# Kernel tuning notes

Hardware: AMD Instinct MI355X
Metric: run time of the kernel (lower is better)

Reference implementation:

```python
import jax, jax.numpy as jnp
import numpy as np

B = 2048   # jets (graphs)
P = 50     # particles per jet
N = B * P  # nodes
E = B * P * P  # within-jet all-pairs radius-graph edges (incl. self-loops)
H = 5      # edge-MLP width ([5,5,5,5] channel list)
EPS = 1e-5
NEG_SLOPE = 0.01


def _batchnorm(h, gamma, beta):
    # training-mode batch norm over the edge dimension (biased variance, as torch)
    mu = jnp.mean(h, axis=0)
    var = jnp.mean(h * h, axis=0) - mu * mu
    return gamma * (h - mu) * jax.lax.rsqrt(var + EPS) + beta


def setup_inputs() -> dict:
    key = jax.random.key(0)
    ks = jax.random.split(key, 16)
    # angles: per-jet center offset + tight spread so all within-jet pairs are inside dR=0.4
    centers = jax.random.normal(ks[0], (B, 1, 2), dtype=jnp.float32) + jnp.array([2.0, 0.5], dtype=jnp.float32)
    angles = (centers + 0.1 * jax.random.normal(ks[1], (B, P, 2), dtype=jnp.float32)).reshape(N, 2)
    pt = jax.random.uniform(ks[2], (N,), dtype=jnp.float32, minval=0.1, maxval=1.0)
    features = jnp.linalg.norm(angles, axis=-1, keepdims=True)  # rho = |view_as_complex(angles)|, [N,1]
    # radius graph: with the tight spread every within-jet pair is within dR -> fixed E
    ii = np.arange(P)
    pi, pj = np.meshgrid(ii, ii, indexing='ij')
    base = (np.arange(B, dtype=np.int64) * P)[:, None]
    src = (base + pj.ravel()[None, :]).ravel()  # x_j (source)
    dst = (base + pi.ravel()[None, :]).ravel()  # x_i (target) = aggregation index
    edge_index = jnp.asarray(np.stack([src, dst]), dtype=jnp.int32)  # [2, E]
    def lin(k, o, i):
        return (jax.random.normal(k, (o, i), dtype=jnp.float32) / np.sqrt(i)).astype(jnp.float32)
    W1 = lin(ks[3], H, 5); b1 = jnp.zeros((H,), jnp.float32)
    W2 = lin(ks[4], H, H); b2 = jnp.zeros((H,), jnp.float32)
    W3 = lin(ks[5], H, H); b3 = jnp.zeros((H,), jnp.float32)
    g1 = jnp.ones((H,), jnp.float32); bt1 = jnp.zeros((H,), jnp.float32)
    g2 = jnp.ones((H,), jnp.float32); bt2 = jnp.zeros((H,), jnp.float32)
    return {"pt": pt, "features": features, "angles": angles,
            "W1": W1, "b1": b1, "g1": g1, "bt1": bt1,
            "W2": W2, "b2": b2, "g2": g2, "bt2": bt2,
            "W3": W3, "b3": b3, "edge_index": edge_index}


def reference(pt, features, angles, W1, b1, g1, bt1, W2, b2, g2, bt2, W3, b3, edge_index):
    src = edge_index[0]  # j (source)
    dst = edge_index[1]  # i (target, aggregation index)
    x = jnp.concatenate([pt[:, None], features, angles], axis=1)  # [N, 4]
    xi = x[dst]  # [E, 4]
    xj = x[src]
    # complex ratio angles_i / angles_j in real arithmetic
    ar, ai = xi[:, 2], xi[:, 3]
    br, bi = xj[:, 2], xj[:, 3]
    den = br * br + bi * bi
    dr = (ar * br + ai * bi) / den
    di = (ai * br - ar * bi) / den
    fi = xi[:, 1:2]
    fj = xj[:, 1:2]
    mlp_in = jnp.concatenate([fi, fj, fj - fi, dr[:, None], di[:, None]], axis=1)  # [E, 5]
    h = jax.nn.leaky_relu(_batchnorm(mlp_in @ W1.T + b1, g1, bt1), NEG_SLOPE)
    h = jax.nn.leaky_relu(_batchnorm(h @ W2.T + b2, g2, bt2), NEG_SLOPE)
    h = h @ W3.T + b3  # [E, 5]
    msg = jnp.concatenate([xi[:, :1], h, xi[:, 2:4]], axis=1)  # [E, 8]
    pt_e = msg[:, 0]
    denom = jax.ops.segment_sum(pt_e, dst, num_segments=N)  # [N]
    wj = pt_e / denom[dst]
    agg = jax.ops.segment_sum(wj[:, None] * msg, dst, num_segments=N)  # [N, 8]
    # exp(2*pi*i*theta) * z with theta = agg[:, -3], z = complex(agg[:, -2:])
    theta = agg[:, 5]
    zr, zi = agg[:, 6], agg[:, 7]
    c = jnp.cos(2.0 * jnp.pi * theta)
    s = jnp.sin(2.0 * jnp.pi * theta)
    out = jnp.concatenate([agg[:, :5], (c * zr - s * zi)[:, None], (c * zi + s * zr)[:, None]], axis=1)  # [N, 7]
    return out
```

## Files before the change

### kernel.cpp

```cpp
#include <hip/hip_runtime.h>

#define PP 50
#define TPB 256
#define NBATCH 2048
#define GB 2
#define NBLK2 (NBATCH / GB)
#define NBLK1 512
#define NCOPY 64
#define NSLOT 30

static constexpr float EPSF = 1e-5f;
static constexpr double INV_ETOT = 1.0 / 5120000.0;

static __device__ __forceinline__ float lrelu(float x) {
    return fmaxf(x, 0.01f * x);
}
static __device__ __forceinline__ float rfl(float x) {
    return __int_as_float(__builtin_amdgcn_readfirstlane(__float_as_int(x)));
}


__global__ __launch_bounds__(TPB) void stats1_kernel(
    const float* __restrict__ feat, const float* __restrict__ ang,
    const float* __restrict__ W1, const float* __restrict__ b1,
    double* __restrict__ acc)
{
    __shared__ double bacc[4][10];
    const int t = threadIdx.x;
    const int lane = t & 63;
    const int wv = t >> 6;

    float v0[5], v1[5], v2[5], v3[5], bb1[5];
#pragma unroll
    for (int o = 0; o < 5; ++o) {
        v0[o] = rfl(W1[o*5+0] - W1[o*5+2]);
        v1[o] = rfl(W1[o*5+1] + W1[o*5+2]);
        v2[o] = rfl(W1[o*5+3]);
        v3[o] = rfl(W1[o*5+4]);
        bb1[o] = rfl(b1[o]);
    }

    float f = 0.f, zr = 0.f, zi = 0.f, inv = 0.f;
    if (lane < PP) {
        const int idx = (blockIdx.x * 4 + wv) * PP + lane;
        f = feat[idx];
        float2 a2 = ((const float2*)ang)[idx];
        zr = a2.x; zi = a2.y;
        inv = 1.0f / (zr*zr + zi*zi);
    }
    const float wr = zr * inv, wi = -zi * inv;

    float p[16] = { f, f*f, zr, zi, wr, wi, f*zr, f*zi, f*wr, f*wi,
                    zr*zr, zi*zi, zr*zi, wr*wr, wi*wi, wr*wi };
#pragma unroll
    for (int k = 0; k < 16; ++k) {
        float v = p[k];
#pragma unroll
        for (int off = 32; off > 0; off >>= 1) v += __shfl_down(v, off, 64);
        p[k] = v;
    }
    if (lane == 0) {
        const double P0 = p[0], P1 = p[1], P2 = p[2], P3 = p[3], P4 = p[4];
        const double P5 = p[5], P6 = p[6], P7 = p[7], P8 = p[8], P9 = p[9];
        const double P10 = p[10], P11 = p[11], P12 = p[12];
        const double P13 = p[13], P14 = p[14], P15 = p[15];
        const double Sfi = 50.0 * P0;
        const double Sdr = P2*P4 - P3*P5;
        const double Sdi = P3*P4 + P2*P5;
        const double m00 = 50.0 * P1, m11 = m00, m01 = P0*P0;
        const double m02 = P6*P4 - P7*P5;
        const double m03 = P7*P4 + P6*P5;
        const double m12 = P2*P8 - P3*P9;
        const double m13 = P3*P8 + P2*P9;
        const double m22 = P10*P13 - 2.0*P12*P15 + P11*P14;
        const double m33 = P11*P13 + 2.0*P12*P15 + P10*P14;
        const double m23 = P12*P13 + P10*P15 - P11*P15 - P12*P14;
#pragma unroll
        for (int o = 0; o < 5; ++o) {
            const double a0=v0[o], a1=v1[o], a2=v2[o], a3=v3[o], bo=bb1[o];
            const double sy = a0*Sfi + a1*Sfi + a2*Sdr + a3*Sdi + 2500.0*bo;
            const double q  = a0*a0*m00 + a1*a1*m11 + a2*a2*m22 + a3*a3*m33
                           + 2.0*(a0*a1*m01 + a0*a2*m02 + a0*a3*m03
                                + a1*a2*m12 + a1*a3*m13 + a2*a3*m23);
            bacc[wv][o]   = sy;
            bacc[wv][5+o] = q + 2.0*bo*sy - 2500.0*bo*bo;
        }
    }
    __syncthreads();
    if (t < 10) {
        double s = bacc[0][t] + bacc[1][t] + bacc[2][t] + bacc[3][t];
        atomicAdd(&acc[t * NCOPY + (blockIdx.x & (NCOPY-1))], s);
    }
}

__global__ __launch_bounds__(TPB, 2) void pass2_kernel(
    const float* __restrict__ feat, const float* __restrict__ ang,
    const float* __restrict__ W1, const float* __restrict__ b1,
    const float* __restrict__ g1, const float* __restrict__ bt1,
    double* __restrict__ acc)
{
    __shared__ float4 nd[GB * PP];
    __shared__ float4 ndj[GB * PP];
    __shared__ double tmp[10];
    __shared__ float red[4][20];
    const int t = threadIdx.x;

    if (t < GB * PP) {
        const int idx = blockIdx.x * (GB * PP) + t;
        float f = feat[idx];
        float2 a2 = ((const float2*)ang)[idx];
        float inv = 1.0f / (a2.x*a2.x + a2.y*a2.y);
        nd[t]  = make_float4(f, a2.x, a2.y, 0.0f);
        ndj[t] = make_float4(f, a2.x * inv, a2.y * inv, 0.0f);
    } else if (t >= 128 && t < 138) {
        const int k = t - 128;
        double s = 0.0;
#pragma unroll
        for (int c = 0; c < NCOPY; ++c) s += acc[k * NCOPY + c];
        tmp[k] = s;
    }

    float v0[5], v1[5], v2[5], v3[5], bb1[5];
#pragma unroll
    for (int o = 0; o < 5; ++o) {
        v0[o] = rfl(W1[o*5+0] - W1[o*5+2]);
        v1[o] = rfl(W1[o*5+1] + W1[o*5+2]);
        v2[o] = rfl(W1[o*5+3]);
        v3[o] = rfl(W1[o*5+4]);
        bb1[o] = rfl(b1[o]);
    }

    __syncthreads();

#pragma unroll
    for (int o = 0; o < 5; ++o) {
        double mu  = tmp[o]   * INV_ETOT;
        double var = tmp[5+o] * INV_ETOT - mu * mu;
        float sc = rfl(g1[o]) * rsqrtf((float)var + EPSF);
        float sh = rfl(rfl(bt1[o]) - (float)mu * sc);
        v0[o] = rfl(v0[o] * sc);
        v1[o] = rfl(v1[o] * sc);
        v2[o] = rfl(v2[o] * sc);
        v3[o] = rfl(v3[o] * sc);
        bb1[o] = rfl(fmaf(bb1[o], sc, sh));
    }

    float s1[5] = {0.f, 0.f, 0.f, 0.f, 0.f};
    float mm[15];
#pragma unroll
    for (int k = 0; k < 15; ++k) mm[k] = 0.f;

    if (t < 250) {
        const int pi = t / 5;
        const int s5 = t - pi*5;
#pragma unroll
        for (int g = 0; g < GB; ++g) {
            const float4 ni = nd[g*PP + pi];
            const float fi = ni.x, ari = ni.y, aii = ni.z;
            float4 njs[10];
#pragma unroll
            for (int q = 0; q < 10; ++q) njs[q] = ndj[g*PP + s5*10 + q];
#pragma unroll
            for (int q = 0; q < 10; ++q) {
                const float4 nj = njs[q];
                const float dr = fmaf(ari, nj.y,  aii*nj.z);
                const float di = fmaf(aii, nj.y, -ari*nj.z);
                float h1[5];
#pragma unroll
                for (int o = 0; o < 5; ++o) {
                    float y = fmaf(v0[o], fi, fmaf(v1[o], nj.x,
                              fmaf(v2[o], dr, fmaf(v3[o], di, bb1[o]))));
                    h1[o] = lrelu(y);
                }
#pragma unroll
                for (int k = 0; k < 5; ++k) {
                    s1[k] += h1[k];
#pragma unroll
                    for (int l = k; l < 5; ++l) {
                        const int idx = k*5 - (k*(k+1))/2 + l;
                        mm[idx] = fmaf(h1[k], h1[l], mm[idx]);
                    }
                }
            }
        }
    }

    float a[20];
#pragma unroll
    for (int k = 0; k < 5; ++k) a[k] = s1[k];
#pragma unroll
    for (int k = 0; k < 15; ++k) a[5+k] = mm[k];
#pragma unroll
    for (int k = 0; k < 20; ++k) {
        float v = a[k];
#pragma unroll
        for (int off = 32; off > 0; off >>= 1) v += __shfl_down(v, off, 64);
        a[k] = v;
    }
    const int lane = t & 63, wv = t >> 6;
    if (lane == 0) {
#pragma unroll
        for (int k = 0; k < 20; ++k) red[wv][k] = a[k];
    }
    __syncthreads();
    if (t < 20) {
        atomicAdd(&acc[(10 + t) * NCOPY + (blockIdx.x & (NCOPY-1))],
                  (double)(red[0][t] + red[1][t] + red[2][t] + red[3][t]));
    }
}

__global__ __launch_bounds__(TPB, 2) void pass3_kernel(
    const float* __restrict__ pt,
    const float* __restrict__ feat, const float* __restrict__ ang,
    const float* __restrict__ W1, const float* __restrict__ b1,
    const float* __restrict__ g1, const float* __restrict__ bt1,
    const float* __restrict__ W2, const float* __restrict__ b2,
    const float* __restrict__ g2, const float* __restrict__ bt2,
    const float* __restrict__ W3, const float* __restrict__ b3,
    const double* __restrict__ acc, float* __restrict__ out)
{
    __shared__ float4 nd[GB * PP];
    __shared__ float4 ndj[GB * PP];
    __shared__ float spt[GB * PP];
    __shared__ double tmp[NSLOT];
    __shared__ float scsh[4][5];
    __shared__ float part[250][5];
    const int t = threadIdx.x;

    if (t < GB * PP) {
        const int idx = blockIdx.x * (GB * PP) + t;
        float f = feat[idx];
        float2 a2 = ((const float2*)ang)[idx];
        float inv = 1.0f / (a2.x*a2.x + a2.y*a2.y);
        nd[t]  = make_float4(f, a2.x, a2.y, 0.0f);
        ndj[t] = make_float4(f, a2.x * inv, a2.y * inv, 0.0f);
        spt[t] = pt[idx];
    } else if (t >= 128 && t < 128 + NSLOT) {
        const int k = t - 128;
        double s = 0.0;
#pragma unroll
        for (int c = 0; c < NCOPY; ++c) s += acc[k * NCOPY + c];
        tmp[k] = s;
    }

    float v0[5], v1[5], v2[5], v3[5], bb1[5], w2[25], bb2[5], w3[25], bb3[5];
#pragma unroll
    for (int o = 0; o < 5; ++o) {
        v0[o] = rfl(W1[o*5+0] - W1[o*5+2]);
        v1[o] = rfl(W1[o*5+1] + W1[o*5+2]);
        v2[o] = rfl(W1[o*5+3]);
        v3[o] = rfl(W1[o*5+4]);
        bb1[o] = rfl(b1[o]); bb2[o] = rfl(b2[o]); bb3[o] = rfl(b3[o]);
    }
#pragma unroll
    for (int i = 0; i < 25; ++i) { w2[i] = rfl(W2[i]); w3[i] = rfl(W3[i]); }

    __syncthreads();

    if (t < 5) {
        const int o = t;
        double mu1  = tmp[o]   * INV_ETOT;
        double var1 = tmp[5+o] * INV_ETOT - mu1 * mu1;
        float sc1 = g1[o] * rsqrtf((float)var1 + EPSF);
        scsh[0][o] = sc1;
        scsh[1][o] = bt1[o] - (float)mu1 * sc1;

        double w[5], Sn[5];
#pragma unroll
        for (int k = 0; k < 5; ++k) {
            w[k]  = (double)w2[o*5+k];
            Sn[k] = tmp[10+k] * INV_ETOT;
        }
        double muw = 0.0;
#pragma unroll
        for (int k = 0; k < 5; ++k) muw += w[k] * Sn[k];
        double q = 0.0;
#pragma unroll
        for (int k = 0; k < 5; ++k) {
#pragma unroll
            for (int l = k; l < 5; ++l) {
                const int idx = k*5 - (k*(k+1))/2 + l;
                const double Mn = tmp[15+idx] * INV_ETOT;
                q += (k == l ? w[k]*w[k] : 2.0*w[k]*w[l]) * Mn;
            }
        }
        double var2 = q - muw * muw;
        double mu2  = muw + (double)bb2[o];
        float sc2 = g2[o] * rsqrtf((float)var2 + EPSF);
        scsh[2][o] = sc2;
        scsh[3][o] = bt2[o] - (float)mu2 * sc2;
    }
    __syncthreads();

#pragma unroll
    for (int o = 0; o < 5; ++o) {
        const float s1f = rfl(scsh[0][o]);
        const float s1h = rfl(scsh[1][o]);
        v0[o] = rfl(v0[o] * s1f);
        v1[o] = rfl(v1[o] * s1f);
        v2[o] = rfl(v2[o] * s1f);
        v3[o] = rfl(v3[o] * s1f);
        bb1[o] = rfl(fmaf(bb1[o], s1f, s1h));
        const float s2f = rfl(scsh[2][o]);
        const float s2h = rfl(scsh[3][o]);
#pragma unroll
        for (int k = 0; k < 5; ++k) w2[o*5+k] = rfl(w2[o*5+k] * s2f);
        bb2[o] = rfl(fmaf(bb2[o], s2f, s2h));
    }

    const int pi = t / 5;
    const int s5 = t - pi*5;

#pragma unroll
    for (int g = 0; g < GB; ++g) {
        float a[5] = {0.f, 0.f, 0.f, 0.f, 0.f};
        if (t < 250) {
            const float4 ni = nd[g*PP + pi];
            const float fi = ni.x, ari = ni.y, aii = ni.z;
            float4 njs[10];
#pragma unroll
            for (int q = 0; q < 10; ++q) njs[q] = ndj[g*PP + s5*10 + q];
#pragma unroll
            for (int q = 0; q < 10; ++q) {
                const float4 nj = njs[q];
                const float dr = fmaf(ari, nj.y,  aii*nj.z);
                const float di = fmaf(aii, nj.y, -ari*nj.z);
                float h1[5], h2[5];
#pragma unroll
                for (int o = 0; o < 5; ++o) {
                    float y = fmaf(v0[o], fi, fmaf(v1[o], nj.x,
                              fmaf(v2[o], dr, fmaf(v3[o], di, bb1[o]))));
                    h1[o] = lrelu(y);
                }
#pragma unroll
                for (int o = 0; o < 5; ++o) {
                    float y = bb2[o];
                    y = fmaf(w2[o*5+0], h1[0], y);
                    y = fmaf(w2[o*5+1], h1[1], y);
                    y = fmaf(w2[o*5+2], h1[2], y);
                    y = fmaf(w2[o*5+3], h1[3], y);
                    y = fmaf(w2[o*5+4], h1[4], y);
                    h2[o] = lrelu(y);
                }
#pragma unroll
                for (int o = 0; o < 5; ++o) a[o] += h2[o];
            }
#pragma unroll
            for (int c = 0; c < 5; ++c) part[t][c] = a[c];
        }
        __syncthreads();

        if (t < PP) {
            float hm[5];
#pragma unroll
            for (int c = 0; c < 5; ++c) {
                hm[c] = (part[5*t][c] + part[5*t+1][c] + part[5*t+2][c] +
                         part[5*t+3][c] + part[5*t+4][c]) * 0.02f;
            }
            float m[5];
#pragma unroll
            for (int c = 0; c < 5; ++c) {
                float y = bb3[c];
                y = fmaf(w3[c*5+0], hm[0], y);
                y = fmaf(w3[c*5+1], hm[1], y);
                y = fmaf(w3[c*5+2], hm[2], y);
                y = fmaf(w3[c*5+3], hm[3], y);
                y = fmaf(w3[c*5+4], hm[4], y);
                m[c] = y;
            }
            const int node = g*PP + t;
            const int d = blockIdx.x * (GB * PP) + node;
            const float4 ni = nd[node];
            float ss, cc;
            sincosf(6.2831853071795865f * m[4], &ss, &cc);
            float* o = out + (size_t)d * 7;
            o[0] = spt[node];
            o[1] = m[0];
            o[2] = m[1];
            o[3] = m[2];
            o[4] = m[3];
            o[5] = cc * ni.y - ss * ni.z;
            o[6] = cc * ni.z + ss * ni.y;
        }
        __syncthreads();
    }
}

extern "C" void kernel_launch(void* const* d_in, const int* in_sizes, int n_in,
                              void* d_out, int out_size, void* d_ws, size_t ws_size,
                              hipStream_t stream)
{
    const float* pt   = (const float*)d_in[0];
    const float* feat = (const float*)d_in[1];
    const float* ang  = (const float*)d_in[2];
    const float* W1   = (const float*)d_in[3];
    const float* b1   = (const float*)d_in[4];
    const float* g1   = (const float*)d_in[5];
    const float* bt1  = (const float*)d_in[6];
    const float* W2   = (const float*)d_in[7];
    const float* b2   = (const float*)d_in[8];
    const float* g2   = (const float*)d_in[9];
    const float* bt2  = (const float*)d_in[10];
    const float* W3   = (const float*)d_in[11];
    const float* b3   = (const float*)d_in[12];
    float* out = (float*)d_out;
    double* acc = (double*)d_ws;

    hipMemsetAsync(d_ws, 0, NSLOT * NCOPY * sizeof(double), stream);
    stats1_kernel<<<NBLK1, TPB, 0, stream>>>(feat, ang, W1, b1, acc);
    pass2_kernel<<<NBLK2, TPB, 0, stream>>>(feat, ang, W1, b1, g1, bt1, acc);
    pass3_kernel<<<NBLK2, TPB, 0, stream>>>(pt, feat, ang, W1, b1, g1, bt1, W2, b2,
                                            g2, bt2, W3, b3, acc, out);
}
```

Before: 140.5 us.

## Fuse three passes into one persistent kernel with grid-wide barriers

Merges the stats, second-moment and output kernels into a single kernel of 512 blocks, each handling four jets, and separates the phases with atomic grid barriers. Node data is staged in shared memory once and reused across all three phases instead of being reloaded per launch, and launch gaps disappear. It relies on all 512 blocks being co-resident (two per CU under the launch bounds); otherwise the spin barrier deadlocks. Fewer blocks also means less parallel slack in each phase.

```diff
diff --git a/kernel.cpp b/kernel.cpp
--- a/kernel.cpp
+++ b/kernel.cpp
@@ -3,10 +3,9 @@
 #define PP 50
 #define TPB 256
 #define NBATCH 2048
-#define GB 2
-#define NBLK2 (NBATCH / GB)
-#define NBLK1 512
-#define NCOPY 64
+#define GBF 4
+#define NBLKF (NBATCH / GBF)
+#define NCOPY 32
 #define NSLOT 30
 
 static constexpr float EPSF = 1e-5f;
@@ -18,17 +17,60 @@
 static __device__ __forceinline__ float rfl(float x) {
     return __int_as_float(__builtin_amdgcn_readfirstlane(__float_as_int(x)));
 }
-
-
-__global__ __launch_bounds__(TPB) void stats1_kernel(
+static __device__ __forceinline__ double aload(const double* p) {
+    return __hip_atomic_load(p, __ATOMIC_RELAXED, __HIP_MEMORY_SCOPE_AGENT);
+}
+
+static __device__ __forceinline__ void gbar(unsigned* cnt, unsigned* gen) {
+    __syncthreads();
+    if (threadIdx.x == 0) {
+        if (__hip_atomic_fetch_add(cnt, 1u, __ATOMIC_ACQ_REL,
+                                   __HIP_MEMORY_SCOPE_AGENT) == NBLKF - 1u) {
+            __hip_atomic_store(gen, 1u, __ATOMIC_RELEASE,
+                               __HIP_MEMORY_SCOPE_AGENT);
+        } else {
+            while (__hip_atomic_load(gen, __ATOMIC_ACQUIRE,
+                                     __HIP_MEMORY_SCOPE_AGENT) == 0u) {
+                __builtin_amdgcn_s_sleep(1);
+            }
+        }
+    }
+    __syncthreads();
+}
+
+__global__ __launch_bounds__(TPB, 2) void fused_kernel(
+    const float* __restrict__ pt,
     const float* __restrict__ feat, const float* __restrict__ ang,
     const float* __restrict__ W1, const float* __restrict__ b1,
-    double* __restrict__ acc)
+    const float* __restrict__ g1, const float* __restrict__ bt1,
+    const float* __restrict__ W2, const float* __restrict__ b2,
+    const float* __restrict__ g2, const float* __restrict__ bt2,
+    const float* __restrict__ W3, const float* __restrict__ b3,
+    double* __restrict__ acc, unsigned* __restrict__ bar,
+    float* __restrict__ out)
 {
+    __shared__ float4 nd[GBF * PP];
+    __shared__ float4 ndj[GBF * PP];
+    __shared__ float spt[GBF * PP];
     __shared__ double bacc[4][10];
+    __shared__ double tmp[NSLOT];
+    __shared__ float scsh[2][5];
+    __shared__ float red[4][20];
+    __shared__ float part[250][5];
+
     const int t = threadIdx.x;
     const int lane = t & 63;
     const int wv = t >> 6;
+
+    if (t < GBF * PP) {
+        const int idx = blockIdx.x * (GBF * PP) + t;
+        float f = feat[idx];
+        float2 a2 = ((const float2*)ang)[idx];
+        float inv = 1.0f / (a2.x * a2.x + a2.y * a2.y);
+        nd[t]  = make_float4(f, a2.x, a2.y, 0.0f);
+        ndj[t] = make_float4(f, a2.x * inv, a2.y * inv, 0.0f);
+        spt[t] = pt[idx];
+    }
 
     float v0[5], v1[5], v2[5], v3[5], bb1[5];
 #pragma unroll
@@ -40,96 +82,69 @@
         bb1[o] = rfl(b1[o]);
     }
 
-    float f = 0.f, zr = 0.f, zi = 0.f, inv = 0.f;
-    if (lane < PP) {
-        const int idx = (blockIdx.x * 4 + wv) * PP + lane;
-        f = feat[idx];
-        float2 a2 = ((const float2*)ang)[idx];
-        zr = a2.x; zi = a2.y;
-        inv = 1.0f / (zr*zr + zi*zi);
-    }
-    const float wr = zr * inv, wi = -zi * inv;
-
-    float p[16] = { f, f*f, zr, zi, wr, wi, f*zr, f*zi, f*wr, f*wi,
-                    zr*zr, zi*zi, zr*zi, wr*wr, wi*wi, wr*wi };
-#pragma unroll
-    for (int k = 0; k < 16; ++k) {
-        float v = p[k];
-#pragma unroll
-        for (int off = 32; off > 0; off >>= 1) v += __shfl_down(v, off, 64);
-        p[k] = v;
-    }
-    if (lane == 0) {
-        const double P0 = p[0], P1 = p[1], P2 = p[2], P3 = p[3], P4 = p[4];
-        const double P5 = p[5], P6 = p[6], P7 = p[7], P8 = p[8], P9 = p[9];
-        const double P10 = p[10], P11 = p[11], P12 = p[12];
-        const double P13 = p[13], P14 = p[14], P15 = p[15];
-        const double Sfi = 50.0 * P0;
-        const double Sdr = P2*P4 - P3*P5;
-        const double Sdi = P3*P4 + P2*P5;
-        const double m00 = 50.0 * P1, m11 = m00, m01 = P0*P0;
-        const double m02 = P6*P4 - P7*P5;
-        const double m03 = P7*P4 + P6*P5;
-        const double m12 = P2*P8 - P3*P9;
-        const double m13 = P3*P8 + P2*P9;
-        const double m22 = P10*P13 - 2.0*P12*P15 + P11*P14;
-        const double m33 = P11*P13 + 2.0*P12*P15 + P10*P14;
-        const double m23 = P12*P13 + P10*P15 - P11*P15 - P12*P14;
-#pragma unroll
-        for (int o = 0; o < 5; ++o) {
-            const double a0=v0[o], a1=v1[o], a2=v2[o], a3=v3[o], bo=bb1[o];
-            const double sy = a0*Sfi + a1*Sfi + a2*Sdr + a3*Sdi + 2500.0*bo;
-            const double q  = a0*a0*m00 + a1*a1*m11 + a2*a2*m22 + a3*a3*m33
-                           + 2.0*(a0*a1*m01 + a0*a2*m02 + a0*a3*m03
-                                + a1*a2*m12 + a1*a3*m13 + a2*a3*m23);
-            bacc[wv][o]   = sy;
-            bacc[wv][5+o] = q + 2.0*bo*sy - 2500.0*bo*bo;
-        }
-    }
-    __syncthreads();
+    __syncthreads();
+
+    {
+        float f = 0.f, zr = 0.f, zi = 0.f, wr = 0.f, wi = 0.f;
+        if (lane < PP) {
+            const int node = wv * PP + lane;
+            const float4 ni = nd[node];
+            const float4 nj = ndj[node];
+            f = ni.x; zr = ni.y; zi = ni.z;
+            wr = nj.y; wi = -nj.z;
+        }
+        float p[16] = { f, f*f, zr, zi, wr, wi, f*zr, f*zi, f*wr, f*wi,
+                        zr*zr, zi*zi, zr*zi, wr*wr, wi*wi, wr*wi };
+#pragma unroll
+        for (int k = 0; k < 16; ++k) {
+            float v = p[k];
+#pragma unroll
+            for (int off = 32; off > 0; off >>= 1) v += __shfl_down(v, off, 64);
+            p[k] = v;
+        }
+        if (lane == 0) {
+            const double P0 = p[0], P1 = p[1], P2 = p[2], P3 = p[3], P4 = p[4];
+            const double P5 = p[5], P6 = p[6], P7 = p[7], P8 = p[8], P9 = p[9];
+            const double P10 = p[10], P11 = p[11], P12 = p[12];
+            const double P13 = p[13], P14 = p[14], P15 = p[15];
+            const double Sfi = 50.0 * P0;
+            const double Sdr = P2*P4 - P3*P5;
+            const double Sdi = P3*P4 + P2*P5;
+            const double m00 = 50.0 * P1, m11 = m00, m01 = P0*P0;
+            const double m02 = P6*P4 - P7*P5;
+            const double m03 = P7*P4 + P6*P5;
+            const double m12 = P2*P8 - P3*P9;
+            const double m13 = P3*P8 + P2*P9;
+            const double m22 = P10*P13 - 2.0*P12*P15 + P11*P14;
+            const double m33 = P11*P13 + 2.0*P12*P15 + P10*P14;
+            const double m23 = P12*P13 + P10*P15 - P11*P15 - P12*P14;
+#pragma unroll
+            for (int o = 0; o < 5; ++o) {
+                const double a0=v0[o], a1=v1[o], a2=v2[o], a3=v3[o], bo=bb1[o];
+                const double sy = a0*Sfi + a1*Sfi + a2*Sdr + a3*Sdi + 2500.0*bo;
+                const double q  = a0*a0*m00 + a1*a1*m11 + a2*a2*m22 + a3*a3*m33
+                               + 2.0*(a0*a1*m01 + a0*a2*m02 + a0*a3*m03
+                                    + a1*a2*m12 + a1*a3*m13 + a2*a3*m23);
+                bacc[wv][o]   = sy;
+                bacc[wv][5+o] = q + 2.0*bo*sy - 2500.0*bo*bo;
+            }
+        }
+    }
+    __syncthreads();
+
     if (t < 10) {
         double s = bacc[0][t] + bacc[1][t] + bacc[2][t] + bacc[3][t];
         atomicAdd(&acc[t * NCOPY + (blockIdx.x & (NCOPY-1))], s);
     }
-}
-
-__global__ __launch_bounds__(TPB, 2) void pass2_kernel(
-    const float* __restrict__ feat, const float* __restrict__ ang,
-    const float* __restrict__ W1, const float* __restrict__ b1,
-    const float* __restrict__ g1, const float* __restrict__ bt1,
-    double* __restrict__ acc)
-{
-    __shared__ float4 nd[GB * PP];
-    __shared__ float4 ndj[GB * PP];
-    __shared__ double tmp[10];
-    __shared__ float red[4][20];
-    const int t = threadIdx.x;
-
-    if (t < GB * PP) {
-        const int idx = blockIdx.x * (GB * PP) + t;
-        float f = feat[idx];
-        float2 a2 = ((const float2*)ang)[idx];
-        float inv = 1.0f / (a2.x*a2.x + a2.y*a2.y);
-        nd[t]  = make_float4(f, a2.x, a2.y, 0.0f);
-        ndj[t] = make_float4(f, a2.x * inv, a2.y * inv, 0.0f);
-    } else if (t >= 128 && t < 138) {
-        const int k = t - 128;
+
+    gbar(&bar[0], &bar[1]);
+
+    if (t < 10) {
         double s = 0.0;
 #pragma unroll
-        for (int c = 0; c < NCOPY; ++c) s += acc[k * NCOPY + c];
-        tmp[k] = s;
-    }
-
-    float v0[5], v1[5], v2[5], v3[5], bb1[5];
-#pragma unroll
-    for (int o = 0; o < 5; ++o) {
-        v0[o] = rfl(W1[o*5+0] - W1[o*5+2]);
-        v1[o] = rfl(W1[o*5+1] + W1[o*5+2]);
-        v2[o] = rfl(W1[o*5+3]);
-        v3[o] = rfl(W1[o*5+4]);
-        bb1[o] = rfl(b1[o]);
-    }
-
+        for (int c = 0; c < NCOPY; ++c) s += aload(&acc[t * NCOPY + c]);
+        tmp[t] = s;
+    }
     __syncthreads();
 
 #pragma unroll
@@ -145,126 +160,89 @@
         bb1[o] = rfl(fmaf(bb1[o], sc, sh));
     }
 
-    float s1[5] = {0.f, 0.f, 0.f, 0.f, 0.f};
-    float mm[15];
-#pragma unroll
-    for (int k = 0; k < 15; ++k) mm[k] = 0.f;
-
-    if (t < 250) {
-        const int pi = t / 5;
-        const int s5 = t - pi*5;
-#pragma unroll
-        for (int g = 0; g < GB; ++g) {
-            const float4 ni = nd[g*PP + pi];
-            const float fi = ni.x, ari = ni.y, aii = ni.z;
-            float4 njs[10];
-#pragma unroll
-            for (int q = 0; q < 10; ++q) njs[q] = ndj[g*PP + s5*10 + q];
-#pragma unroll
-            for (int q = 0; q < 10; ++q) {
-                const float4 nj = njs[q];
-                const float dr = fmaf(ari, nj.y,  aii*nj.z);
-                const float di = fmaf(aii, nj.y, -ari*nj.z);
-                float h1[5];
-#pragma unroll
-                for (int o = 0; o < 5; ++o) {
-                    float y = fmaf(v0[o], fi, fmaf(v1[o], nj.x,
-                              fmaf(v2[o], dr, fmaf(v3[o], di, bb1[o]))));
-                    h1[o] = lrelu(y);
-                }
-#pragma unroll
-                for (int k = 0; k < 5; ++k) {
-                    s1[k] += h1[k];
-#pragma unroll
-                    for (int l = k; l < 5; ++l) {
-                        const int idx = k*5 - (k*(k+1))/2 + l;
-                        mm[idx] = fmaf(h1[k], h1[l], mm[idx]);
+    const int pi = t / 5;
+    const int s5 = t - pi * 5;
+
+    {
+        float s1[5] = {0.f, 0.f, 0.f, 0.f, 0.f};
+        float mm[15];
+#pragma unroll
+        for (int k = 0; k < 15; ++k) mm[k] = 0.f;
+
+        if (t < 250) {
+#pragma unroll
+            for (int g = 0; g < GBF; ++g) {
+                const float4 ni = nd[g*PP + pi];
+                const float fi = ni.x, ari = ni.y, aii = ni.z;
+                float4 njs[10];
+#pragma unroll
+                for (int q = 0; q < 10; ++q) njs[q] = ndj[g*PP + s5*10 + q];
+#pragma unroll
+                for (int q = 0; q < 10; ++q) {
+                    const float4 nj = njs[q];
+                    const float dr = fmaf(ari, nj.y,  aii*nj.z);
+                    const float di = fmaf(aii, nj.y, -ari*nj.z);
+                    float h1[5];
+#pragma unroll
+                    for (int o = 0; o < 5; ++o) {
+                        float y = fmaf(v0[o], fi, fmaf(v1[o], nj.x,
+                                  fmaf(v2[o], dr, fmaf(v3[o], di, bb1[o]))));
+                        h1[o] = lrelu(y);
+                    }
+#pragma unroll
+                    for (int k = 0; k < 5; ++k) {
+                        s1[k] += h1[k];
+#pragma unroll
+                        for (int l = k; l < 5; ++l) {
+                            const int idx = k*5 - (k*(k+1))/2 + l;
+                            mm[idx] = fmaf(h1[k], h1[l], mm[idx]);
+                        }
                     }
                 }
             }
         }
-    }
-
-    float a[20];
-#pragma unroll
-    for (int k = 0; k < 5; ++k) a[k] = s1[k];
-#pragma unroll
-    for (int k = 0; k < 15; ++k) a[5+k] = mm[k];
-#pragma unroll
-    for (int k = 0; k < 20; ++k) {
-        float v = a[k];
-#pragma unroll
-        for (int off = 32; off > 0; off >>= 1) v += __shfl_down(v, off, 64);
-        a[k] = v;
-    }
-    const int lane = t & 63, wv = t >> 6;
-    if (lane == 0) {
-#pragma unroll
-        for (int k = 0; k < 20; ++k) red[wv][k] = a[k];
+
+        float a[20];
+#pragma unroll
+        for (int k = 0; k < 5; ++k) a[k] = s1[k];
+#pragma unroll
+        for (int k = 0; k < 15; ++k) a[5+k] = mm[k];
+#pragma unroll
+        for (int k = 0; k < 20; ++k) {
+            float v = a[k];
+#pragma unroll
+            for (int off = 32; off > 0; off >>= 1) v += __shfl_down(v, off, 64);
+            a[k] = v;
+        }
+        if (lane == 0) {
+#pragma unroll
+            for (int k = 0; k < 20; ++k) red[wv][k] = a[k];
+        }
     }
     __syncthreads();
     if (t < 20) {
         atomicAdd(&acc[(10 + t) * NCOPY + (blockIdx.x & (NCOPY-1))],
                   (double)(red[0][t] + red[1][t] + red[2][t] + red[3][t]));
     }
-}
-
-__global__ __launch_bounds__(TPB, 2) void pass3_kernel(
-    const float* __restrict__ pt,
-    const float* __restrict__ feat, const float* __restrict__ ang,
-    const float* __restrict__ W1, const float* __restrict__ b1,
-    const float* __restrict__ g1, const float* __restrict__ bt1,
-    const float* __restrict__ W2, const float* __restrict__ b2,
-    const float* __restrict__ g2, const float* __restrict__ bt2,
-    const float* __restrict__ W3, const float* __restrict__ b3,
-    const double* __restrict__ acc, float* __restrict__ out)
-{
-    __shared__ float4 nd[GB * PP];
-    __shared__ float4 ndj[GB * PP];
-    __shared__ float spt[GB * PP];
-    __shared__ double tmp[NSLOT];
-    __shared__ float scsh[4][5];
-    __shared__ float part[250][5];
-    const int t = threadIdx.x;
-
-    if (t < GB * PP) {
-        const int idx = blockIdx.x * (GB * PP) + t;
-        float f = feat[idx];
-        float2 a2 = ((const float2*)ang)[idx];
-        float inv = 1.0f / (a2.x*a2.x + a2.y*a2.y);
-        nd[t]  = make_float4(f, a2.x, a2.y, 0.0f);
-        ndj[t] = make_float4(f, a2.x * inv, a2.y * inv, 0.0f);
-        spt[t] = pt[idx];
-    } else if (t >= 128 && t < 128 + NSLOT) {
-        const int k = t - 128;
+
+    gbar(&bar[2], &bar[3]);
+
+    if (t < 20) {
         double s = 0.0;
 #pragma unroll
-        for (int c = 0; c < NCOPY; ++c) s += acc[k * NCOPY + c];
-        tmp[k] = s;
-    }
-
-    float v0[5], v1[5], v2[5], v3[5], bb1[5], w2[25], bb2[5], w3[25], bb3[5];
-#pragma unroll
-    for (int o = 0; o < 5; ++o) {
-        v0[o] = rfl(W1[o*5+0] - W1[o*5+2]);
-        v1[o] = rfl(W1[o*5+1] + W1[o*5+2]);
-        v2[o] = rfl(W1[o*5+3]);
-        v3[o] = rfl(W1[o*5+4]);
-        bb1[o] = rfl(b1[o]); bb2[o] = rfl(b2[o]); bb3[o] = rfl(b3[o]);
-    }
-#pragma unroll
-    for (int i = 0; i < 25; ++i) { w2[i] = rfl(W2[i]); w3[i] = rfl(W3[i]); }
-
+        for (int c = 0; c < NCOPY; ++c) s += aload(&acc[(10 + t) * NCOPY + c]);
+        tmp[10 + t] = s;
+    }
+
+    float w2[25], bb2[5];
+#pragma unroll
+    for (int i = 0; i < 25; ++i) w2[i] = rfl(W2[i]);
+#pragma unroll
+    for (int o = 0; o < 5; ++o) bb2[o] = rfl(b2[o]);
     __syncthreads();
 
     if (t < 5) {
         const int o = t;
-        double mu1  = tmp[o]   * INV_ETOT;
-        double var1 = tmp[5+o] * INV_ETOT - mu1 * mu1;
-        float sc1 = g1[o] * rsqrtf((float)var1 + EPSF);
-        scsh[0][o] = sc1;
-        scsh[1][o] = bt1[o] - (float)mu1 * sc1;
-
         double w[5], Sn[5];
 #pragma unroll
         for (int k = 0; k < 5; ++k) {
@@ -287,32 +265,28 @@
         double var2 = q - muw * muw;
         double mu2  = muw + (double)bb2[o];
         float sc2 = g2[o] * rsqrtf((float)var2 + EPSF);
-        scsh[2][o] = sc2;
-        scsh[3][o] = bt2[o] - (float)mu2 * sc2;
+        scsh[0][o] = sc2;
+        scsh[1][o] = bt2[o] - (float)mu2 * sc2;
     }
     __syncthreads();
 
 #pragma unroll
     for (int o = 0; o < 5; ++o) {
-        const float s1f = rfl(scsh[0][o]);
-        const float s1h = rfl(scsh[1][o]);
-        v0[o] = rfl(v0[o] * s1f);
-        v1[o] = rfl(v1[o] * s1f);
-        v2[o] = rfl(v2[o] * s1f);
-        v3[o] = rfl(v3[o] * s1f);
-        bb1[o] = rfl(fmaf(bb1[o], s1f, s1h));
-        const float s2f = rfl(scsh[2][o]);
-        const float s2h = rfl(scsh[3][o]);
+        const float s2f = rfl(scsh[0][o]);
+        const float s2h = rfl(scsh[1][o]);
 #pragma unroll
         for (int k = 0; k < 5; ++k) w2[o*5+k] = rfl(w2[o*5+k] * s2f);
         bb2[o] = rfl(fmaf(bb2[o], s2f, s2h));
     }
 
-    const int pi = t / 5;
-    const int s5 = t - pi*5;
-
-#pragma unroll
-    for (int g = 0; g < GB; ++g) {
+    float w3[25], bb3[5];
+#pragma unroll
+    for (int i = 0; i < 25; ++i) w3[i] = rfl(W3[i]);
+#pragma unroll
+    for (int o = 0; o < 5; ++o) bb3[o] = rfl(b3[o]);
+
+#pragma unroll
+    for (int g = 0; g < GBF; ++g) {
         float a[5] = {0.f, 0.f, 0.f, 0.f, 0.f};
         if (t < 250) {
             const float4 ni = nd[g*PP + pi];
@@ -369,7 +343,7 @@
                 m[c] = y;
             }
             const int node = g*PP + t;
-            const int d = blockIdx.x * (GB * PP) + node;
+            const int d = blockIdx.x * (GBF * PP) + node;
             const float4 ni = nd[node];
             float ss, cc;
             sincosf(6.2831853071795865f * m[4], &ss, &cc);
@@ -405,10 +379,11 @@
     const float* b3   = (const float*)d_in[12];
     float* out = (float*)d_out;
     double* acc = (double*)d_ws;
-
-    hipMemsetAsync(d_ws, 0, NSLOT * NCOPY * sizeof(double), stream);
-    stats1_kernel<<<NBLK1, TPB, 0, stream>>>(feat, ang, W1, b1, acc);
-    pass2_kernel<<<NBLK2, TPB, 0, stream>>>(feat, ang, W1, b1, g1, bt1, acc);
-    pass3_kernel<<<NBLK2, TPB, 0, stream>>>(pt, feat, ang, W1, b1, g1, bt1, W2, b2,
-                                            g2, bt2, W3, b3, acc, out);
-}
+    unsigned* bar = (unsigned*)(acc + NSLOT * NCOPY);
+
+    hipMemsetAsync(d_ws, 0, NSLOT * NCOPY * sizeof(double) + 4 * sizeof(unsigned),
+                   stream);
+    fused_kernel<<<NBLKF, TPB, 0, stream>>>(pt, feat, ang, W1, b1, g1, bt1,
+                                            W2, b2, g2, bt2, W3, b3,
+                                            acc, bar, out);
+}
```

Result: slower. 200.2 us (+42.5%).

## Drop memset launch, write stats1 per-block partials, stage output through LDS

Applied to the files above, without the earlier changes.

Removes the separate hipMemsetAsync by having block 0 of stats1 zero the pass2 accumulator. stats1 now writes per-block partial sums to a workspace array instead of doing atomics, and pass2/pass3 reduce those 512 partials in a two-level shared-memory tree. Pass3 stages each jet's 7-float outputs in LDS and writes them out as coalesced float2 stores. NCOPY for the remaining atomics is halved. The partial reads add work to every pass2/pass3 block in exchange for one fewer launch and less atomic contention.

```diff
diff --git a/kernel.cpp b/kernel.cpp
--- a/kernel.cpp
+++ b/kernel.cpp
@@ -6,8 +6,7 @@
 #define GB 2
 #define NBLK2 (NBATCH / GB)
 #define NBLK1 512
-#define NCOPY 64
-#define NSLOT 30
+#define NCOPY 32
 
 static constexpr float EPSF = 1e-5f;
 static constexpr double INV_ETOT = 1.0 / 5120000.0;
@@ -18,17 +17,20 @@
 static __device__ __forceinline__ float rfl(float x) {
     return __int_as_float(__builtin_amdgcn_readfirstlane(__float_as_int(x)));
 }
-
 
 __global__ __launch_bounds__(TPB) void stats1_kernel(
     const float* __restrict__ feat, const float* __restrict__ ang,
     const float* __restrict__ W1, const float* __restrict__ b1,
-    double* __restrict__ acc)
+    double* __restrict__ acc, double* __restrict__ pacc)
 {
     __shared__ double bacc[4][10];
     const int t = threadIdx.x;
     const int lane = t & 63;
     const int wv = t >> 6;
+
+    if (blockIdx.x == 0) {
+        for (int i = t; i < 20 * NCOPY; i += TPB) acc[i] = 0.0;
+    }
 
     float v0[5], v1[5], v2[5], v3[5], bb1[5];
 #pragma unroll
@@ -88,8 +90,8 @@
     }
     __syncthreads();
     if (t < 10) {
-        double s = bacc[0][t] + bacc[1][t] + bacc[2][t] + bacc[3][t];
-        atomicAdd(&acc[t * NCOPY + (blockIdx.x & (NCOPY-1))], s);
+        pacc[t * NBLK1 + blockIdx.x] =
+            bacc[0][t] + bacc[1][t] + bacc[2][t] + bacc[3][t];
     }
 }
 
@@ -97,11 +99,12 @@
     const float* __restrict__ feat, const float* __restrict__ ang,
     const float* __restrict__ W1, const float* __restrict__ b1,
     const float* __restrict__ g1, const float* __restrict__ bt1,
-    double* __restrict__ acc)
+    double* __restrict__ acc, const double* __restrict__ pacc)
 {
     __shared__ float4 nd[GB * PP];
     __shared__ float4 ndj[GB * PP];
     __shared__ double tmp[10];
+    __shared__ double pred[10][16];
     __shared__ float red[4][20];
     const int t = threadIdx.x;
 
@@ -112,12 +115,12 @@
         float inv = 1.0f / (a2.x*a2.x + a2.y*a2.y);
         nd[t]  = make_float4(f, a2.x, a2.y, 0.0f);
         ndj[t] = make_float4(f, a2.x * inv, a2.y * inv, 0.0f);
-    } else if (t >= 128 && t < 138) {
-        const int k = t - 128;
+    } else if (t >= 100 && t < 250) {
+        const int r = t - 100;
+        const int slot = r / 15, sub = r - slot * 15;
         double s = 0.0;
-#pragma unroll
-        for (int c = 0; c < NCOPY; ++c) s += acc[k * NCOPY + c];
-        tmp[k] = s;
+        for (int b = sub; b < NBLK1; b += 15) s += pacc[slot * NBLK1 + b];
+        pred[slot][sub] = s;
     }
 
     float v0[5], v1[5], v2[5], v3[5], bb1[5];
@@ -130,6 +133,13 @@
         bb1[o] = rfl(b1[o]);
     }
 
+    __syncthreads();
+    if (t < 10) {
+        double s = 0.0;
+#pragma unroll
+        for (int k = 0; k < 15; ++k) s += pred[t][k];
+        tmp[t] = s;
+    }
     __syncthreads();
 
 #pragma unroll
@@ -204,7 +214,7 @@
     }
     __syncthreads();
     if (t < 20) {
-        atomicAdd(&acc[(10 + t) * NCOPY + (blockIdx.x & (NCOPY-1))],
+        atomicAdd(&acc[t * NCOPY + (blockIdx.x & (NCOPY-1))],
                   (double)(red[0][t] + red[1][t] + red[2][t] + red[3][t]));
     }
 }
@@ -217,14 +227,17 @@
     const float* __restrict__ W2, const float* __restrict__ b2,
     const float* __restrict__ g2, const float* __restrict__ bt2,
     const float* __restrict__ W3, const float* __restrict__ b3,
-    const double* __restrict__ acc, float* __restrict__ out)
+    const double* __restrict__ acc, const double* __restrict__ pacc,
+    float* __restrict__ out)
 {
     __shared__ float4 nd[GB * PP];
     __shared__ float4 ndj[GB * PP];
     __shared__ float spt[GB * PP];
-    __shared__ double tmp[NSLOT];
-    __shared__ float scsh[4][5];
+    __shared__ double tmp[30];
+    __shared__ double pred[10][16];
+    __shared__ float scsh[2][5];
     __shared__ float part[250][5];
+    __shared__ __align__(16) float ob[PP * 7 + 2];
     const int t = threadIdx.x;
 
     if (t < GB * PP) {
@@ -235,12 +248,18 @@
         nd[t]  = make_float4(f, a2.x, a2.y, 0.0f);
         ndj[t] = make_float4(f, a2.x * inv, a2.y * inv, 0.0f);
         spt[t] = pt[idx];
-    } else if (t >= 128 && t < 128 + NSLOT) {
-        const int k = t - 128;
+    }
+    if (t < 20) {
         double s = 0.0;
 #pragma unroll
-        for (int c = 0; c < NCOPY; ++c) s += acc[k * NCOPY + c];
-        tmp[k] = s;
+        for (int c = 0; c < NCOPY; ++c) s += acc[t * NCOPY + c];
+        tmp[10 + t] = s;
+    } else if (t >= 100 && t < 250) {
+        const int r = t - 100;
+        const int slot = r / 15, sub = r - slot * 15;
+        double s = 0.0;
+        for (int b = sub; b < NBLK1; b += 15) s += pacc[slot * NBLK1 + b];
+        pred[slot][sub] = s;
     }
 
     float v0[5], v1[5], v2[5], v3[5], bb1[5], w2[25], bb2[5], w3[25], bb3[5];
@@ -256,15 +275,29 @@
     for (int i = 0; i < 25; ++i) { w2[i] = rfl(W2[i]); w3[i] = rfl(W3[i]); }
 
     __syncthreads();
+    if (t < 10) {
+        double s = 0.0;
+#pragma unroll
+        for (int k = 0; k < 15; ++k) s += pred[t][k];
+        tmp[t] = s;
+    }
+    __syncthreads();
+
+#pragma unroll
+    for (int o = 0; o < 5; ++o) {
+        double mu  = tmp[o]   * INV_ETOT;
+        double var = tmp[5+o] * INV_ETOT - mu * mu;
+        float sc = rfl(g1[o]) * rsqrtf((float)var + EPSF);
+        float sh = rfl(rfl(bt1[o]) - (float)mu * sc);
+        v0[o] = rfl(v0[o] * sc);
+        v1[o] = rfl(v1[o] * sc);
+        v2[o] = rfl(v2[o] * sc);
+        v3[o] = rfl(v3[o] * sc);
+        bb1[o] = rfl(fmaf(bb1[o], sc, sh));
+    }
 
     if (t < 5) {
         const int o = t;
-        double mu1  = tmp[o]   * INV_ETOT;
-        double var1 = tmp[5+o] * INV_ETOT - mu1 * mu1;
-        float sc1 = g1[o] * rsqrtf((float)var1 + EPSF);
-        scsh[0][o] = sc1;
-        scsh[1][o] = bt1[o] - (float)mu1 * sc1;
-
         double w[5], Sn[5];
 #pragma unroll
         for (int k = 0; k < 5; ++k) {
@@ -287,22 +320,15 @@
         double var2 = q - muw * muw;
         double mu2  = muw + (double)bb2[o];
         float sc2 = g2[o] * rsqrtf((float)var2 + EPSF);
-        scsh[2][o] = sc2;
-        scsh[3][o] = bt2[o] - (float)mu2 * sc2;
-    }
-    __syncthreads();
-
-#pragma unroll
-    for (int o = 0; o < 5; ++o) {
-        const float s1f = rfl(scsh[0][o]);
-        const float s1h = rfl(scsh[1][o]);
-        v0[o] = rfl(v0[o] * s1f);
-        v1[o] = rfl(v1[o] * s1f);
-        v2[o] = rfl(v2[o] * s1f);
-        v3[o] = rfl(v3[o] * s1f);
-        bb1[o] = rfl(fmaf(bb1[o], s1f, s1h));
-        const float s2f = rfl(scsh[2][o]);
-        const float s2h = rfl(scsh[3][o]);
+        scsh[0][o] = sc2;
+        scsh[1][o] = bt2[o] - (float)mu2 * sc2;
+    }
+    __syncthreads();
+
+#pragma unroll
+    for (int o = 0; o < 5; ++o) {
+        const float s2f = rfl(scsh[0][o]);
+        const float s2h = rfl(scsh[1][o]);
 #pragma unroll
         for (int k = 0; k < 5; ++k) w2[o*5+k] = rfl(w2[o*5+k] * s2f);
         bb2[o] = rfl(fmaf(bb2[o], s2f, s2h));
@@ -369,11 +395,10 @@
                 m[c] = y;
             }
             const int node = g*PP + t;
-            const int d = blockIdx.x * (GB * PP) + node;
             const float4 ni = nd[node];
             float ss, cc;
             sincosf(6.2831853071795865f * m[4], &ss, &cc);
-            float* o = out + (size_t)d * 7;
+            float* o = &ob[t * 7];
             o[0] = spt[node];
             o[1] = m[0];
             o[2] = m[1];
@@ -381,6 +406,13 @@
             o[4] = m[3];
             o[5] = cc * ni.y - ss * ni.z;
             o[6] = cc * ni.z + ss * ni.y;
+        }
+        __syncthreads();
+
+        if (t < 175) {
+            float2* dst = (float2*)(out +
+                (size_t)(blockIdx.x * (GB * PP) + g * PP) * 7);
+            dst[t] = ((const float2*)ob)[t];
         }
         __syncthreads();
     }
@@ -404,11 +436,12 @@
     const float* W3   = (const float*)d_in[11];
     const float* b3   = (const float*)d_in[12];
     float* out = (float*)d_out;
-    double* acc = (double*)d_ws;
-
-    hipMemsetAsync(d_ws, 0, NSLOT * NCOPY * sizeof(double), stream);
-    stats1_kernel<<<NBLK1, TPB, 0, stream>>>(feat, ang, W1, b1, acc);
-    pass2_kernel<<<NBLK2, TPB, 0, stream>>>(feat, ang, W1, b1, g1, bt1, acc);
-    pass3_kernel<<<NBLK2, TPB, 0, stream>>>(pt, feat, ang, W1, b1, g1, bt1, W2, b2,
-                                            g2, bt2, W3, b3, acc, out);
-}
+    double* acc  = (double*)d_ws;
+    double* pacc = acc + 20 * NCOPY;
+
+    stats1_kernel<<<NBLK1, TPB, 0, stream>>>(feat, ang, W1, b1, acc, pacc);
+    pass2_kernel<<<NBLK2, TPB, 0, stream>>>(feat, ang, W1, b1, g1, bt1, acc, pacc);
+    pass3_kernel<<<NBLK2, TPB, 0, stream>>>(pt, feat, ang, W1, b1, g1, bt1,
+                                            W2, b2, g2, bt2, W3, b3,
+                                            acc, pacc, out);
+}
```

Result: slower. 152.2 us (+8.3%).
